# Optimization experiments

Hardware: AMD Instinct MI355X
Metric: run time of the kernel (lower is better)

The kernel has to match this reference:

```python
import jax, jax.numpy as jnp
import numpy as np

N_NODES = 100000
N_EDGES = 1600000
D = 128


def setup_inputs() -> dict:
    key = jax.random.key(0)
    ks = jax.random.split(key, 10)
    features = jax.random.normal(ks[0], (N_NODES, D), dtype=jnp.float32)
    edge_index = jax.random.randint(ks[1], (2, N_EDGES), 0, N_NODES, dtype=jnp.int64)
    edge_weight = jax.random.uniform(ks[2], (N_EDGES,), dtype=jnp.float32)
    scale = 1.0 / np.sqrt(D)
    W1 = jax.random.normal(ks[3], (D, D), dtype=jnp.float32) * scale
    b1 = jnp.zeros((D,), dtype=jnp.float32)
    a1 = jnp.full((D,), 0.25, dtype=jnp.float32)  # PReLU init
    W2 = jax.random.normal(ks[4], (D, D), dtype=jnp.float32) * scale
    b2 = jnp.zeros((D,), dtype=jnp.float32)
    a2 = jnp.full((D,), 0.25, dtype=jnp.float32)
    return {"features": features, "edge_index": edge_index, "edge_weight": edge_weight,
            "W1": W1, "b1": b1, "a1": a1, "W2": W2, "b2": b2, "a2": a2}


def _gcn_norm(edge_index, edge_weight, n_nodes):
    # PyG GCNConv default: add self-loops (weight 1), symmetric normalization.
    src, dst = edge_index[0], edge_index[1]
    loop = jnp.arange(n_nodes, dtype=src.dtype)
    src = jnp.concatenate([src, loop])
    dst = jnp.concatenate([dst, loop])
    w = jnp.concatenate([edge_weight, jnp.ones((n_nodes,), edge_weight.dtype)])
    deg = jax.ops.segment_sum(w, dst, num_segments=n_nodes)  # in-degree (target)
    dis = jnp.where(deg > 0, jax.lax.rsqrt(deg), 0.0)
    norm = dis[src] * w * dis[dst]  # [E + N]
    return src, dst, norm


def _gcn_layer(x, W, b, src, dst, norm, n_nodes):
    h = x @ W                                 # [N, D] dense GEMM first (PyG order)
    msg = h[src] * norm[:, None]              # gather + scale, [E+N, D]
    out = jax.ops.segment_sum(msg, dst, num_segments=n_nodes)
    return out + b


def _prelu(x, a):
    return jnp.where(x >= 0, x, a * x)


def reference(features, edge_index, edge_weight, W1, b1, a1, W2, b2, a2):
    n = features.shape[0]
    src, dst, norm = _gcn_norm(edge_index, edge_weight, n)
    # dropout is identity in eval mode
    x = _prelu(_gcn_layer(features, W1, b1, src, dst, norm, n), a1)
    x = _prelu(_gcn_layer(x, W2, b2, src, dst, norm, n), a2)
    return x
```

## Files before the change

kernel.cpp:

```cpp
#include <hip/hip_runtime.h>
#include <cstdint>

#define NN 100000
#define NE 1600000
#define DD 128
#define NB 250
#define BSZ 400
#define NHB ((NE + 8191) / 8192)

typedef unsigned int uint;
typedef unsigned short ushort;
typedef unsigned long long u64;

typedef __attribute__((ext_vector_type(8))) short short8;
typedef __attribute__((ext_vector_type(4))) float floatx4;

__device__ inline uint f2bf(float f) {
    uint u = __float_as_uint(f);
    return (u + 0x7fffu + ((u >> 16) & 1u)) >> 16;
}


__global__ __launch_bounds__(256) void bucket_hist(const int* __restrict__ dst,
                                                   uint* __restrict__ bcp) {
    __shared__ uint h[NB];
    int tid = threadIdx.x;
    if (tid < NB) h[tid] = 0u;
    __syncthreads();
    int e0 = blockIdx.x * 8192 + tid;
#pragma unroll
    for (int k = 0; k < 32; ++k) {
        int e = e0 + 256 * k;
        if (e < NE) atomicAdd(&h[(uint)dst[e] / BSZ], 1u);
    }
    __syncthreads();
    if (tid < NB) bcp[blockIdx.x * 256 + tid] = h[tid];
}

__global__ __launch_bounds__(256) void bucket_prefix(const uint* __restrict__ bcp,
                                                     uint* __restrict__ bbase,
                                                     uint* __restrict__ bcur) {
    __shared__ uint cnt[NB];
    int tid = threadIdx.x;
    if (tid < NB) {
        uint s = 0;
        for (int j = 0; j < NHB; ++j) s += bcp[j * 256 + tid];
        cnt[tid] = s;
    }
    __syncthreads();
    int lane = tid;
    if (lane < 64) {
        uint v[4], s = 0;
#pragma unroll
        for (int k = 0; k < 4; ++k) {
            int i = lane * 4 + k;
            v[k] = (i < NB) ? cnt[i] : 0u;
            s += v[k];
        }
        uint inc = s;
#pragma unroll
        for (int d = 1; d < 64; d <<= 1) {
            uint t = __shfl_up(inc, (unsigned)d, 64);
            if (lane >= d) inc += t;
        }
        uint run = inc - s;
#pragma unroll
        for (int k = 0; k < 4; ++k) {
            int i = lane * 4 + k;
            if (i < NB) { bbase[i] = run; bcur[i] = run; run += v[k]; }
        }
        if (lane == 63) bbase[NB] = run;
    }
}

__global__ __launch_bounds__(256) void bucket_append(const int* __restrict__ src,
                                                     const int* __restrict__ dst,
                                                     const float* __restrict__ w,
                                                     uint* __restrict__ bcur,
                                                     int2* __restrict__ etmp) {
    __shared__ uint h[NB];
    __shared__ uint res[NB];
    int tid = threadIdx.x;
    if (tid < NB) h[tid] = 0u;
    __syncthreads();
    int e0 = blockIdx.x * 4096 + tid;
    uint rank[16], bkt[16];
#pragma unroll
    for (int k = 0; k < 16; ++k) {
        int e = e0 + 256 * k;
        if (e < NE) {
            uint b = (uint)dst[e] / BSZ;
            bkt[k] = b;
            rank[k] = atomicAdd(&h[b], 1u);
        } else bkt[k] = 0xffffffffu;
    }
    __syncthreads();
    if (tid < NB) res[tid] = h[tid] ? atomicAdd(&bcur[tid], h[tid]) : 0u;
    __syncthreads();
#pragma unroll
    for (int k = 0; k < 16; ++k) {
        if (bkt[k] != 0xffffffffu) {
            int e = e0 + 256 * k;
            uint dl = (uint)dst[e] - bkt[k] * BSZ;
            uint wq = (uint)(w[e] * 8388608.0f);
            if (wq > 8388607u) wq = 8388607u;
            etmp[res[bkt[k]] + rank[k]] = make_int2(src[e], (int)((dl << 23) | wq));
        }
    }
}

__global__ __launch_bounds__(256) void bucket_build(const int2* __restrict__ etmp,
                                                    const uint* __restrict__ bbase,
                                                    float* __restrict__ dis,
                                                    int* __restrict__ hist_g,
                                                    int* __restrict__ rowstart,
                                                    int2* __restrict__ edges) {
    __shared__ u64   wc[BSZ];
    __shared__ uint  cur[BSZ];
    __shared__ float disl[BSZ];
    int tid = threadIdx.x;
    int b = blockIdx.x;
    int n0 = b * BSZ;
    for (int i = tid; i < BSZ; i += 256) wc[i] = 0ull;
    __syncthreads();
    uint base = bbase[b], end = bbase[b + 1];
    for (uint i = base + tid; i < end; i += 256) {
        uint y = (uint)etmp[i].y;
        uint dl = y >> 23;
        atomicAdd(&wc[dl], ((u64)1 << 40) | (u64)(y & 0x7fffffu));
    }
    __syncthreads();
    if (tid < 64) {
        uint v[7], s = 0;
#pragma unroll
        for (int k = 0; k < 7; ++k) {
            int i = tid * 7 + k;
            v[k] = (i < BSZ) ? (uint)(wc[i] >> 40) : 0u;
            s += v[k];
        }
        uint inc = s;
#pragma unroll
        for (int d = 1; d < 64; d <<= 1) {
            uint t = __shfl_up(inc, (unsigned)d, 64);
            if (tid >= d) inc += t;
        }
        uint run = inc - s;
#pragma unroll
        for (int k = 0; k < 7; ++k) {
            int i = tid * 7 + k;
            if (i < BSZ) { cur[i] = run; run += v[k]; }
        }
    }
    __syncthreads();
    for (int i = tid; i < BSZ; i += 256) {
        u64 v = wc[i];
        float wsum = (float)(v & 0xffffffffffull) * (1.0f / 8388608.0f);
        float ds = rsqrtf(1.0f + wsum);
        disl[i] = ds;
        dis[n0 + i] = ds;
        hist_g[n0 + i] = (int)(v >> 40);
        rowstart[n0 + i] = (int)(base + cur[i]);
    }
    __syncthreads();
    for (uint i = base + tid; i < end; i += 256) {
        int2 e = etmp[i];
        uint y = (uint)e.y;
        uint dl = y >> 23;
        float wv = (float)(y & 0x7fffffu) * (1.0f / 8388608.0f);
        uint p = atomicAdd(&cur[dl], 1u);
        float nrm = wv * disl[dl];
        edges[base + p] = make_int2(e.x, __float_as_int(nrm));
    }
}

#define WTS 136
#define NTILES ((NN + 63) / 64)

template <bool AF32>
__global__ __launch_bounds__(256) void gemm_mfma(const void* __restrict__ Xv,
                                                 const float* __restrict__ W,
                                                 const float* __restrict__ dis,
                                                 ushort* __restrict__ HB) {
    __shared__ ushort Wt[DD * WTS];
    int tid = threadIdx.x;
#pragma unroll
    for (int it = 0; it < 16; ++it) {
        int flat = (tid + it * 256) * 4;
        int k = flat >> 7, n = flat & 127;
        float4 wv = *(const float4*)&W[flat];
        Wt[(n + 0) * WTS + k] = (ushort)f2bf(wv.x);
        Wt[(n + 1) * WTS + k] = (ushort)f2bf(wv.y);
        Wt[(n + 2) * WTS + k] = (ushort)f2bf(wv.z);
        Wt[(n + 3) * WTS + k] = (ushort)f2bf(wv.w);
    }
    __syncthreads();

    int wave = tid >> 6, lane = tid & 63;
    int q = lane >> 4, l16 = lane & 15;

    for (int tile = blockIdx.x; tile < NTILES; tile += gridDim.x) {
        int row0 = tile * 64 + wave * 16;

        int arow = row0 + l16;
        if (arow >= NN) arow = NN - 1;
        short8 afr[4];
        if (AF32) {
            const float* xr = (const float*)Xv + (size_t)arow * DD + q * 8;
#pragma unroll
            for (int ks = 0; ks < 4; ++ks) {
                float4 f0 = *(const float4*)(xr + ks * 32);
                float4 f1 = *(const float4*)(xr + ks * 32 + 4);
                uint4 u;
                u.x = f2bf(f0.x) | (f2bf(f0.y) << 16);
                u.y = f2bf(f0.z) | (f2bf(f0.w) << 16);
                u.z = f2bf(f1.x) | (f2bf(f1.y) << 16);
                u.w = f2bf(f1.z) | (f2bf(f1.w) << 16);
                afr[ks] = __builtin_bit_cast(short8, u);
            }
        } else {
            const ushort* xr = (const ushort*)Xv + (size_t)arow * DD + q * 8;
#pragma unroll
            for (int ks = 0; ks < 4; ++ks)
                afr[ks] = *(const short8*)(xr + ks * 32);
        }

        floatx4 acc[8];
#pragma unroll
        for (int ct = 0; ct < 8; ++ct) acc[ct] = (floatx4)(0.0f);

#pragma unroll
        for (int ct = 0; ct < 8; ++ct) {
            const ushort* wp = &Wt[(ct * 16 + l16) * WTS + q * 8];
#pragma unroll
            for (int ks = 0; ks < 4; ++ks) {
                short8 bfr = *(const short8*)(wp + ks * 32);
                acc[ct] = __builtin_amdgcn_mfma_f32_16x16x32_bf16(afr[ks], bfr, acc[ct], 0, 0, 0);
            }
        }

#pragma unroll
        for (int reg = 0; reg < 4; ++reg) {
            int r = row0 + q * 4 + reg;
            if (r < NN) {
                float ds = dis[r];
                ushort* orow = HB + (size_t)r * DD + l16;
#pragma unroll
                for (int ct = 0; ct < 8; ++ct)
                    orow[ct * 16] = (ushort)f2bf(acc[ct][reg] * ds);
            }
        }
    }
}

template <bool BF16OUT>
__global__ __launch_bounds__(256) void gather_finalize(const ushort* __restrict__ hb,
                                                       const int2* __restrict__ edges,
                                                       const int* __restrict__ rowstart,
                                                       const int* __restrict__ hist,
                                                       const float* __restrict__ dis,
                                                       const float* __restrict__ b,
                                                       const float* __restrict__ a,
                                                       void* __restrict__ xout) {
    int wid = __builtin_amdgcn_readfirstlane(threadIdx.x >> 6);
    int lane = threadIdx.x & 63;
    int nodeA = blockIdx.x * 8 + wid * 2;
    int nodeB = nodeA + 1;
    uint lane4 = (uint)lane * 4u;
    const char* hbase = (const char*)hb;

    int rsA  = rowstart[nodeA];
    int rsB  = rowstart[nodeB];
    int cntA = hist[nodeA];
    int cntB = hist[nodeB];
    float dsA = dis[nodeA];
    float dsB = dis[nodeB];
    const int2* epA = edges + rsA;
    const int2* epB = edges + rsB;

    uint suA = *(const uint*)(hbase + ((size_t)(uint)nodeA << 8) + lane4);
    uint suB = *(const uint*)(hbase + ((size_t)(uint)nodeB << 8) + lane4);
    float2 a0, a1, a2, a3, b0, b1, b2, b3;
    a0.x = __uint_as_float(suA << 16) * dsA;
    a0.y = __uint_as_float(suA & 0xffff0000u) * dsA;
    b0.x = __uint_as_float(suB << 16) * dsB;
    b0.y = __uint_as_float(suB & 0xffff0000u) * dsB;
    a1 = make_float2(0.f, 0.f); a2 = a1; a3 = a1;
    b1 = a1; b2 = a1; b3 = a1;

    int nbA = (cntA + 15) >> 4;
    int nbB = (cntB + 15) >> 4;
    int nb = nbA > nbB ? nbA : nbB;

    for (int t = 0; t < nb; ++t) {
        int remA = cntA - t * 16;
        int remB = cntB - t * 16;
        int2 eA[16], eB[16];
#pragma unroll
        for (int k = 0; k < 16; ++k) eA[k] = epA[t * 16 + k];
#pragma unroll
        for (int k = 0; k < 16; ++k) eB[k] = epB[t * 16 + k];

        uint gA[16], gB[16];
        float nA[16], nB[16];
#pragma unroll
        for (int k = 0; k < 16; ++k) {
            bool live = k < remA;
            uint s = live ? (uint)eA[k].x : 0u;
            nA[k] = live ? __int_as_float(eA[k].y) : 0.0f;
            gA[k] = *(const uint*)(hbase + ((size_t)s << 8) + lane4);
        }
#pragma unroll
        for (int k = 0; k < 16; ++k) {
            bool live = k < remB;
            uint s = live ? (uint)eB[k].x : 0u;
            nB[k] = live ? __int_as_float(eB[k].y) : 0.0f;
            gB[k] = *(const uint*)(hbase + ((size_t)s << 8) + lane4);
        }
#pragma unroll
        for (int k = 0; k < 16; ++k) {
            float2* ac = (k & 3) == 0 ? &a0 : (k & 3) == 1 ? &a1 : (k & 3) == 2 ? &a2 : &a3;
            ac->x += __uint_as_float(gA[k] << 16) * nA[k];
            ac->y += __uint_as_float(gA[k] & 0xffff0000u) * nA[k];
        }
#pragma unroll
        for (int k = 0; k < 16; ++k) {
            float2* ac = (k & 3) == 0 ? &b0 : (k & 3) == 1 ? &b1 : (k & 3) == 2 ? &b2 : &b3;
            ac->x += __uint_as_float(gB[k] << 16) * nB[k];
            ac->y += __uint_as_float(gB[k] & 0xffff0000u) * nB[k];
        }
    }

    float2 bb = ((const float2*)b)[lane];
    float2 aa = ((const float2*)a)[lane];
    float rA0 = a0.x + a1.x + a2.x + a3.x + bb.x;
    float rA1 = a0.y + a1.y + a2.y + a3.y + bb.y;
    float rB0 = b0.x + b1.x + b2.x + b3.x + bb.x;
    float rB1 = b0.y + b1.y + b2.y + b3.y + bb.y;
    rA0 = rA0 >= 0.f ? rA0 : aa.x * rA0;
    rA1 = rA1 >= 0.f ? rA1 : aa.y * rA1;
    rB0 = rB0 >= 0.f ? rB0 : aa.x * rB0;
    rB1 = rB1 >= 0.f ? rB1 : aa.y * rB1;
    if (BF16OUT) {
        ((uint*)xout)[(size_t)nodeA * 64 + lane] = f2bf(rA0) | (f2bf(rA1) << 16);
        ((uint*)xout)[(size_t)nodeB * 64 + lane] = f2bf(rB0) | (f2bf(rB1) << 16);
    } else {
        float2 oA; oA.x = rA0; oA.y = rA1;
        float2 oB; oB.x = rB0; oB.y = rB1;
        ((float2*)xout)[(size_t)nodeA * 64 + lane] = oA;
        ((float2*)xout)[(size_t)nodeB * 64 + lane] = oB;
    }
}

extern "C" void kernel_launch(void* const* d_in, const int* in_sizes, int n_in,
                              void* d_out, int out_size, void* d_ws, size_t ws_size,
                              hipStream_t stream) {
    const float* feat = (const float*)d_in[0];
    const int*   ei   = (const int*)d_in[1];
    const float* ew   = (const float*)d_in[2];
    const float* W1   = (const float*)d_in[3];
    const float* b1   = (const float*)d_in[4];
    const float* a1   = (const float*)d_in[5];
    const float* W2   = (const float*)d_in[6];
    const float* b2   = (const float*)d_in[7];
    const float* a2   = (const float*)d_in[8];
    float* out = (float*)d_out;

    const int* srcp = ei;
    const int* dstp = ei + NE;

    char* wsb = (char*)d_ws;
    size_t off = 0;
    uint* bcp    = (uint*)(wsb + off); off += 4ull * 256 * NHB;
    uint* bbase  = (uint*)(wsb + off); off += 4096;
    uint* bcur   = (uint*)(wsb + off); off += 4096;
    float* dis   = (float*)(wsb + off); off += 4ull * NN;
    int* hist    = (int*)(wsb + off); off += 4ull * NN;
    int* rowstart= (int*)(wsb + off); off += 4ull * NN;
    int2* etmp   = (int2*)(wsb + off); off += 8ull * NE;
    int2* edges  = (int2*)(wsb + off); off += 8ull * NE;
    ushort* hb   = (ushort*)(wsb + off); off += 2ull * NN * DD;
    ushort* x1b  = (ushort*)(wsb + off); off += 2ull * NN * DD;

    bucket_hist<<<NHB, 256, 0, stream>>>(dstp, bcp);
    bucket_prefix<<<1, 256, 0, stream>>>(bcp, bbase, bcur);
    bucket_append<<<(NE + 4095) / 4096, 256, 0, stream>>>(srcp, dstp, ew, bcur, etmp);
    bucket_build<<<NB, 256, 0, stream>>>(etmp, bbase, dis, hist, rowstart, edges);

    const int gemm_blocks = (NTILES + 1) / 2;
    const int gath_blocks = NN / 8;

    gemm_mfma<true><<<gemm_blocks, 256, 0, stream>>>(feat, W1, dis, hb);
    gather_finalize<true><<<gath_blocks, 256, 0, stream>>>(hb, edges, rowstart, hist, dis, b1, a1, x1b);
    gemm_mfma<false><<<gemm_blocks, 256, 0, stream>>>(x1b, W2, dis, hb);
    gather_finalize<false><<<gath_blocks, 256, 0, stream>>>(hb, edges, rowstart, hist, dis, b2, a2, out);
}
```

Before: 368.9 us.

## Pre-transpose weights, transpose bucket histogram, widen bucket_build, split gather launches

Adds a prep kernel that converts and transposes W1/W2 to bf16 once, so each GEMM block only copies short8 vectors into LDS instead of converting and scattering floats. The bucket histogram is stored bucket-major so the prefix kernel can read contiguous uint4 runs. bucket_build now runs with 1024 threads per block for more parallelism per bucket. Each gather_finalize is split into two half-size launches over node ranges. This adds an extra kernel launch and two more gather launches, and the split may only add overhead.

```diff
diff --git a/kernel.cpp b/kernel.cpp
--- a/kernel.cpp
+++ b/kernel.cpp
@@ -20,6 +20,18 @@
     return (u + 0x7fffu + ((u >> 16) & 1u)) >> 16;
 }
 
+__global__ __launch_bounds__(256) void prep_w(const float* __restrict__ W1,
+                                              const float* __restrict__ W2,
+                                              ushort* __restrict__ Wt1,
+                                              ushort* __restrict__ Wt2) {
+    int t = blockIdx.x * 256 + threadIdx.x;
+    if (t < DD * DD) {
+        int k = t >> 7, n = t & 127;
+        Wt1[n * DD + k] = (ushort)f2bf(W1[t]);
+        Wt2[n * DD + k] = (ushort)f2bf(W2[t]);
+    }
+}
+
 
 __global__ __launch_bounds__(256) void bucket_hist(const int* __restrict__ dst,
                                                    uint* __restrict__ bcp) {
@@ -34,7 +46,7 @@
         if (e < NE) atomicAdd(&h[(uint)dst[e] / BSZ], 1u);
     }
     __syncthreads();
-    if (tid < NB) bcp[blockIdx.x * 256 + tid] = h[tid];
+    if (tid < NB) bcp[(size_t)tid * NHB + blockIdx.x] = h[tid];
 }
 
 __global__ __launch_bounds__(256) void bucket_prefix(const uint* __restrict__ bcp,
@@ -43,8 +55,13 @@
     __shared__ uint cnt[NB];
     int tid = threadIdx.x;
     if (tid < NB) {
+        const uint4* p = (const uint4*)(bcp + (size_t)tid * NHB);
         uint s = 0;
-        for (int j = 0; j < NHB; ++j) s += bcp[j * 256 + tid];
+#pragma unroll 7
+        for (int j = 0; j < NHB / 4; ++j) {
+            uint4 v = p[j];
+            s += v.x + v.y + v.z + v.w;
+        }
         cnt[tid] = s;
     }
     __syncthreads();
@@ -109,22 +126,22 @@
     }
 }
 
-__global__ __launch_bounds__(256) void bucket_build(const int2* __restrict__ etmp,
-                                                    const uint* __restrict__ bbase,
-                                                    float* __restrict__ dis,
-                                                    int* __restrict__ hist_g,
-                                                    int* __restrict__ rowstart,
-                                                    int2* __restrict__ edges) {
+__global__ __launch_bounds__(1024) void bucket_build(const int2* __restrict__ etmp,
+                                                     const uint* __restrict__ bbase,
+                                                     float* __restrict__ dis,
+                                                     int* __restrict__ hist_g,
+                                                     int* __restrict__ rowstart,
+                                                     int2* __restrict__ edges) {
     __shared__ u64   wc[BSZ];
     __shared__ uint  cur[BSZ];
     __shared__ float disl[BSZ];
     int tid = threadIdx.x;
     int b = blockIdx.x;
     int n0 = b * BSZ;
-    for (int i = tid; i < BSZ; i += 256) wc[i] = 0ull;
+    for (int i = tid; i < BSZ; i += 1024) wc[i] = 0ull;
     __syncthreads();
     uint base = bbase[b], end = bbase[b + 1];
-    for (uint i = base + tid; i < end; i += 256) {
+    for (uint i = base + tid; i < end; i += 1024) {
         uint y = (uint)etmp[i].y;
         uint dl = y >> 23;
         atomicAdd(&wc[dl], ((u64)1 << 40) | (u64)(y & 0x7fffffu));
@@ -152,7 +169,7 @@
         }
     }
     __syncthreads();
-    for (int i = tid; i < BSZ; i += 256) {
+    for (int i = tid; i < BSZ; i += 1024) {
         u64 v = wc[i];
         float wsum = (float)(v & 0xffffffffffull) * (1.0f / 8388608.0f);
         float ds = rsqrtf(1.0f + wsum);
@@ -162,7 +179,7 @@
         rowstart[n0 + i] = (int)(base + cur[i]);
     }
     __syncthreads();
-    for (uint i = base + tid; i < end; i += 256) {
+    for (uint i = base + tid; i < end; i += 1024) {
         int2 e = etmp[i];
         uint y = (uint)e.y;
         uint dl = y >> 23;
@@ -178,20 +195,17 @@
 
 template <bool AF32>
 __global__ __launch_bounds__(256) void gemm_mfma(const void* __restrict__ Xv,
-                                                 const float* __restrict__ W,
+                                                 const ushort* __restrict__ Wtg,
                                                  const float* __restrict__ dis,
                                                  ushort* __restrict__ HB) {
     __shared__ ushort Wt[DD * WTS];
     int tid = threadIdx.x;
 #pragma unroll
-    for (int it = 0; it < 16; ++it) {
-        int flat = (tid + it * 256) * 4;
-        int k = flat >> 7, n = flat & 127;
-        float4 wv = *(const float4*)&W[flat];
-        Wt[(n + 0) * WTS + k] = (ushort)f2bf(wv.x);
-        Wt[(n + 1) * WTS + k] = (ushort)f2bf(wv.y);
-        Wt[(n + 2) * WTS + k] = (ushort)f2bf(wv.z);
-        Wt[(n + 3) * WTS + k] = (ushort)f2bf(wv.w);
+    for (int u = 0; u < 8; ++u) {
+        int unit = tid + u * 256;
+        int n = unit >> 4, c = unit & 15;
+        short8 v = *(const short8*)(Wtg + n * DD + c * 8);
+        *(short8*)&Wt[n * WTS + c * 8] = v;
     }
     __syncthreads();
 
@@ -260,10 +274,11 @@
                                                        const float* __restrict__ dis,
                                                        const float* __restrict__ b,
                                                        const float* __restrict__ a,
+                                                       int node0,
                                                        void* __restrict__ xout) {
     int wid = __builtin_amdgcn_readfirstlane(threadIdx.x >> 6);
     int lane = threadIdx.x & 63;
-    int nodeA = blockIdx.x * 8 + wid * 2;
+    int nodeA = node0 + blockIdx.x * 8 + wid * 2;
     int nodeB = nodeA + 1;
     uint lane4 = (uint)lane * 4u;
     const char* hbase = (const char*)hb;
@@ -370,7 +385,9 @@
 
     char* wsb = (char*)d_ws;
     size_t off = 0;
-    uint* bcp    = (uint*)(wsb + off); off += 4ull * 256 * NHB;
+    uint* bcp    = (uint*)(wsb + off); off += 262144;
+    ushort* wt1  = (ushort*)(wsb + off); off += 2ull * DD * DD;
+    ushort* wt2  = (ushort*)(wsb + off); off += 2ull * DD * DD;
     uint* bbase  = (uint*)(wsb + off); off += 4096;
     uint* bcur   = (uint*)(wsb + off); off += 4096;
     float* dis   = (float*)(wsb + off); off += 4ull * NN;
@@ -381,16 +398,19 @@
     ushort* hb   = (ushort*)(wsb + off); off += 2ull * NN * DD;
     ushort* x1b  = (ushort*)(wsb + off); off += 2ull * NN * DD;
 
+    prep_w<<<64, 256, 0, stream>>>(W1, W2, wt1, wt2);
     bucket_hist<<<NHB, 256, 0, stream>>>(dstp, bcp);
     bucket_prefix<<<1, 256, 0, stream>>>(bcp, bbase, bcur);
     bucket_append<<<(NE + 4095) / 4096, 256, 0, stream>>>(srcp, dstp, ew, bcur, etmp);
-    bucket_build<<<NB, 256, 0, stream>>>(etmp, bbase, dis, hist, rowstart, edges);
+    bucket_build<<<NB, 1024, 0, stream>>>(etmp, bbase, dis, hist, rowstart, edges);
 
     const int gemm_blocks = (NTILES + 1) / 2;
-    const int gath_blocks = NN / 8;
-
-    gemm_mfma<true><<<gemm_blocks, 256, 0, stream>>>(feat, W1, dis, hb);
-    gather_finalize<true><<<gath_blocks, 256, 0, stream>>>(hb, edges, rowstart, hist, dis, b1, a1, x1b);
-    gemm_mfma<false><<<gemm_blocks, 256, 0, stream>>>(x1b, W2, dis, hb);
-    gather_finalize<false><<<gath_blocks, 256, 0, stream>>>(hb, edges, rowstart, hist, dis, b2, a2, out);
-}
+    const int gath_blocks = NN / 16;
+
+    gemm_mfma<true><<<gemm_blocks, 256, 0, stream>>>(feat, wt1, dis, hb);
+    gather_finalize<true><<<gath_blocks, 256, 0, stream>>>(hb, edges, rowstart, hist, dis, b1, a1, 0, x1b);
+    gather_finalize<true><<<gath_blocks, 256, 0, stream>>>(hb, edges, rowstart, hist, dis, b1, a1, NN / 2, x1b);
+    gemm_mfma<false><<<gemm_blocks, 256, 0, stream>>>(x1b, wt2, dis, hb);
+    gather_finalize<false><<<gath_blocks, 256, 0, stream>>>(hb, edges, rowstart, hist, dis, b2, a2, 0, out);
+    gather_finalize<false><<<gath_blocks, 256, 0, stream>>>(hb, edges, rowstart, hist, dis, b2, a2, NN / 2, out);
+}
```

After: 359.9 us. 2.4% less time.
